# Optimization experiments

Measured on AMD Instinct MI355X. Metric: run time of the kernel, lower is better.

Reference implementation:

```python
import jax, jax.numpy as jnp
import numpy as np

UNITS = 256

def _lstm_step(carry, idx, kernel, rec_kernel, bias, num_chars):
    h, c = carry
    x = jax.nn.one_hot(idx, num_chars, dtype=h.dtype)          # [B, num_chars]
    z = x @ kernel + h @ rec_kernel + bias                      # [B, 4*UNITS]
    i, f, g, o = jnp.split(z, 4, axis=-1)                       # Keras gate order i,f,c,o
    i = jax.nn.sigmoid(i)
    f = jax.nn.sigmoid(f)
    g = jnp.tanh(g)
    o = jax.nn.sigmoid(o)
    c_new = f * c + i * g
    h_new = o * jnp.tanh(c_new)
    return (h_new, c_new), None


def setup_inputs() -> dict:
    key = jax.random.key(0)
    ks = jax.random.split(key, 4)
    num_chars, batch, seq_len = 128, 1024, 512
    x = jax.random.randint(ks[0], (batch, seq_len), 0, num_chars, dtype=jnp.int32)
    kernel = jax.random.normal(ks[1], (num_chars, 4 * UNITS), dtype=jnp.float32) * 0.05
    rec_kernel = jax.random.normal(ks[2], (UNITS, 4 * UNITS), dtype=jnp.float32) * 0.05
    bias = jnp.zeros((4 * UNITS,), dtype=jnp.float32)
    dense_w = jax.random.normal(ks[3], (UNITS, num_chars), dtype=jnp.float32) * 0.05
    dense_b = jnp.zeros((num_chars,), dtype=jnp.float32)
    return {"x": x, "kernel": kernel, "rec_kernel": rec_kernel, "bias": bias,
            "dense_w": dense_w, "dense_b": dense_b}


def reference(x, kernel, rec_kernel, bias, dense_w, dense_b):
    batch = x.shape[0]
    num_chars = kernel.shape[0]
    h0 = jnp.zeros((batch, UNITS), dtype=kernel.dtype)
    c0 = jnp.zeros((batch, UNITS), dtype=kernel.dtype)
    step = lambda carry, idx: _lstm_step(carry, idx, kernel, rec_kernel, bias, num_chars)
    (h, _), _ = jax.lax.scan(step, (h0, c0), x.T)  # scan over time: [S, B]
    logits = h @ dense_w + dense_b                  # [B, num_chars]
    return jax.nn.softmax(logits, axis=-1)
```

## Files before the change

kernel.cpp:

```cpp
#include <hip/hip_runtime.h>
#include <cstdint>

typedef __bf16 bf16x8 __attribute__((ext_vector_type(8)));
typedef float  f32x4  __attribute__((ext_vector_type(4)));

union U4B { uint4 u; bf16x8 b; };
__device__ __forceinline__ bf16x8 as_bf(uint4 u) { U4B x; x.u = u; return x.b; }

__device__ __forceinline__ unsigned short f2b(float x) {
  unsigned int u = __float_as_uint(x);
  unsigned int r = (u + 0x7fffu + ((u >> 16) & 1u)) >> 16;
  return (unsigned short)r;
}
__device__ __forceinline__ float b2f(unsigned int bits_lo16) {
  return __uint_as_float(bits_lo16 << 16);
}

__device__ __forceinline__ float sigm(float x) {
  float e = __builtin_amdgcn_exp2f(x * -1.4426950408889634f);
  return __builtin_amdgcn_rcpf(1.0f + e);
}
__device__ __forceinline__ float tanh_fast(float x) {
  float e = __builtin_amdgcn_exp2f(x * 2.8853900817779268f);
  return 1.0f - 2.0f * __builtin_amdgcn_rcpf(e + 1.0f);
}

__global__ void prep_kernel(const float* __restrict__ rec,
                            const float* __restrict__ kern,
                            const float* __restrict__ bias,
                            const float* __restrict__ dw,
                            unsigned short* __restrict__ recT,
                            unsigned short* __restrict__ kb2,
                            unsigned short* __restrict__ dwT) {
  int id = blockIdx.x * 256 + threadIdx.x;
  if (id < 262144) {
    int colp = id >> 8, k = id & 255;
    int u = colp >> 2, g = colp & 3;
    recT[colp * 256 + k] = f2b(rec[k * 1024 + u + 256 * g]);
  } else if (id < 262144 + 131072) {
    int i = id - 262144;
    int ch = i >> 10, colp = i & 1023;
    int u = colp >> 2, g = colp & 3;
    int oc = u + 256 * g;
    kb2[ch * 1024 + colp] = f2b(kern[ch * 1024 + oc] + bias[oc]);
  } else {
    int i = id - 262144 - 131072;
    int cls = i >> 8, k = i & 255;
    dwT[cls * 256 + k] = f2b(dw[k * 128 + cls]);
  }
}

__global__ __launch_bounds__(512, 2) void lstm_kernel(
    const unsigned short* __restrict__ recT,
    const unsigned short* __restrict__ kb2,
    const unsigned short* __restrict__ dwT,
    const int* __restrict__ x,
    const float* __restrict__ dense_b,
    float* __restrict__ out) {
  __shared__ uint4 A_lds[2][8][512];
  __shared__ unsigned short h_buf[2][16][264];

  const int tid   = threadIdx.x;
  const int lane  = tid & 63;
  const int wid   = tid >> 6;
  const int row16 = lane & 15;
  const int kg    = lane >> 4;
  const int rbase = blockIdx.x << 4;

  const unsigned short* recBase = recT + ((wid * 128 + row16) * 256 + kg * 8);

  uint4 af[4][8];
#pragma unroll
  for (int m = 0; m < 4; ++m)
#pragma unroll
    for (int k = 0; k < 8; ++k) {
      af[m][k] = *(const uint4*)(recBase + m * 4096 + k * 32);
      asm volatile("" : "+v"(af[m][k].x), "+v"(af[m][k].y),
                        "+v"(af[m][k].z), "+v"(af[m][k].w));
    }

#pragma unroll
  for (int s = 0; s < 2; ++s)
#pragma unroll
    for (int k = 0; k < 8; ++k)
      A_lds[s][k][wid * 64 + lane] = *(const uint4*)(recBase + (4 + s) * 4096 + k * 32);

  const unsigned short* sb6 = recBase + 6 * 4096;
  const unsigned short* sb7 = recBase + 7 * 4096;
  uint4 st6[8], st7[8];
#pragma unroll
  for (int k = 0; k < 3; ++k) {
    st6[k] = *(const uint4*)(sb6 + k * 32);
    st7[k] = *(const uint4*)(sb7 + k * 32);
  }

  for (int e = tid; e < 16 * 264; e += 512) (&h_buf[0][0][0])[e] = 0;

  float c_state[8];
#pragma unroll
  for (int m = 0; m < 8; ++m) c_state[m] = 0.0f;

  const int* xrow = x + (rbase + row16) * 512;
  int idx_cur = xrow[0];

  __syncthreads();

  int cur = 0;
  const unsigned aoff_base = (wid * 64 + lane) * 16;

#pragma unroll 1
  for (int t = 0; t < 512; ++t) {
    unsigned z6 = 0, zL = 0;
    asm volatile("" : "+v"(z6), "+v"(zL));
    const unsigned short* sb6v = sb6 + z6;
    const unsigned short* sb7v = sb7 + z6;
    const unsigned aoff = aoff_base + zL;

    int idx_next = xrow[(t + 1 < 512) ? t + 1 : 511];

    const unsigned short* hrow = &h_buf[cur][row16][0];
    const unsigned short* kb = kb2 + (idx_cur * 1024 + wid * 128 + kg * 4);
    uint2 kq[8];

    f32x4 acc[8];
#pragma unroll
    for (int m = 0; m < 8; ++m) acc[m] = f32x4{0.f, 0.f, 0.f, 0.f};

#pragma unroll
    for (int k = 0; k < 8; ++k) {
      uint4 hf = *(const uint4*)(hrow + k * 32 + kg * 8);
      acc[0] = __builtin_amdgcn_mfma_f32_16x16x32_bf16(as_bf(af[0][k]), as_bf(hf), acc[0], 0, 0, 0);
      acc[1] = __builtin_amdgcn_mfma_f32_16x16x32_bf16(as_bf(af[1][k]), as_bf(hf), acc[1], 0, 0, 0);
      acc[2] = __builtin_amdgcn_mfma_f32_16x16x32_bf16(as_bf(af[2][k]), as_bf(hf), acc[2], 0, 0, 0);
      acc[3] = __builtin_amdgcn_mfma_f32_16x16x32_bf16(as_bf(af[3][k]), as_bf(hf), acc[3], 0, 0, 0);
      uint4 a4 = *(const uint4*)((const char*)A_lds + (0 * 8 + k) * 8192 + aoff);
      acc[4] = __builtin_amdgcn_mfma_f32_16x16x32_bf16(as_bf(a4), as_bf(hf), acc[4], 0, 0, 0);
      uint4 a5 = *(const uint4*)((const char*)A_lds + (1 * 8 + k) * 8192 + aoff);
      acc[5] = __builtin_amdgcn_mfma_f32_16x16x32_bf16(as_bf(a5), as_bf(hf), acc[5], 0, 0, 0);
      acc[6] = __builtin_amdgcn_mfma_f32_16x16x32_bf16(as_bf(st6[k]), as_bf(hf), acc[6], 0, 0, 0);
      acc[7] = __builtin_amdgcn_mfma_f32_16x16x32_bf16(as_bf(st7[k]), as_bf(hf), acc[7], 0, 0, 0);
      const int kp = (k + 3) & 7;
      st6[kp] = *(const uint4*)(sb6v + kp * 32);
      st7[kp] = *(const uint4*)(sb7v + kp * 32);
      if (k == 4) {
#pragma unroll
        for (int m = 0; m < 8; ++m) kq[m] = *(const uint2*)(kb + m * 16);
      }
    }

    unsigned short* hn = &h_buf[cur ^ 1][row16][wid * 32 + kg];
#pragma unroll
    for (int m = 0; m < 8; ++m) {
      float zi = acc[m][0] + b2f(kq[m].x & 0xffffu);
      float zf = acc[m][1] + b2f(kq[m].x >> 16);
      float zg = acc[m][2] + b2f(kq[m].y & 0xffffu);
      float zo = acc[m][3] + b2f(kq[m].y >> 16);
      float gi = sigm(zi);
      float gf = sigm(zf);
      float gg = tanh_fast(zg);
      float go = sigm(zo);
      float c  = gf * c_state[m] + gi * gg;
      c_state[m] = c;
      float h  = go * tanh_fast(c);
      hn[m * 4] = f2b(h);
    }
    __syncthreads();
    cur ^= 1;
    idx_cur = idx_next;
  }

  float (*l_lds)[132] = (float (*)[132])A_lds;
  {
    const unsigned short* dwBase = dwT + ((wid * 16 + row16) * 256 + kg * 8);
    uint4 hf[8];
#pragma unroll
    for (int k = 0; k < 8; ++k)
      hf[k] = *(const uint4*)&h_buf[0][row16][k * 32 + kg * 8];
    f32x4 la = {0.f, 0.f, 0.f, 0.f};
#pragma unroll
    for (int k = 0; k < 8; ++k) {
      uint4 afd = *(const uint4*)(dwBase + k * 32);
      la = __builtin_amdgcn_mfma_f32_16x16x32_bf16(as_bf(afd), as_bf(hf[k]), la, 0, 0, 0);
    }
#pragma unroll
    for (int r = 0; r < 4; ++r) {
      int cls = wid * 16 + kg * 4 + r;
      l_lds[row16][cls] = la[r] + dense_b[cls];
    }
  }
  __syncthreads();

  {
    int r = tid >> 5, cg = tid & 31;
    float4 v = *(const float4*)&l_lds[r][cg * 4];
    float mx = fmaxf(fmaxf(v.x, v.y), fmaxf(v.z, v.w));
#pragma unroll
    for (int s = 1; s < 32; s <<= 1) mx = fmaxf(mx, __shfl_xor(mx, s));
    const float L2E = 1.4426950408889634f;
    float e0 = __builtin_amdgcn_exp2f((v.x - mx) * L2E);
    float e1 = __builtin_amdgcn_exp2f((v.y - mx) * L2E);
    float e2 = __builtin_amdgcn_exp2f((v.z - mx) * L2E);
    float e3 = __builtin_amdgcn_exp2f((v.w - mx) * L2E);
    float sm = e0 + e1 + e2 + e3;
#pragma unroll
    for (int s = 1; s < 32; s <<= 1) sm += __shfl_xor(sm, s);
    float inv = __builtin_amdgcn_rcpf(sm);
    float4 o = {e0 * inv, e1 * inv, e2 * inv, e3 * inv};
    *(float4*)&out[(rbase + r) * 128 + cg * 4] = o;
  }
}

extern "C" void kernel_launch(void* const* d_in, const int* in_sizes, int n_in,
                              void* d_out, int out_size, void* d_ws, size_t ws_size,
                              hipStream_t stream) {
  const int*   x      = (const int*)d_in[0];
  const float* kern   = (const float*)d_in[1];
  const float* rec    = (const float*)d_in[2];
  const float* bias   = (const float*)d_in[3];
  const float* dw     = (const float*)d_in[4];
  const float* db     = (const float*)d_in[5];
  float* outp = (float*)d_out;

  unsigned char* ws = (unsigned char*)d_ws;
  unsigned short* recT = (unsigned short*)(ws);
  unsigned short* kb2  = (unsigned short*)(ws + 524288);
  unsigned short* dwT  = (unsigned short*)(ws + 786432);

  prep_kernel<<<1664, 256, 0, stream>>>(rec, kern, bias, dw, recT, kb2, dwT);
  lstm_kernel<<<64, 512, 0, stream>>>(recT, kb2, dwT, x, db, outp);
}
```

Baseline: 2.824 ms.

## Split LSTM step into two half-gate phases overlapping activations with MFMA

Each timestep's gate GEMM is split into two groups of four MFMA accumulators: the first half (register-resident weights) runs, and its gate activations run before the second half (LDS- and streamed weights) is issued, so transcendental work can overlap with matrix work. Input-projection rows for the next timestep are now prefetched a step ahead, and the streamed weight slices are reloaded on a new schedule (upper half at loop top, lower half during the second MFMA phase). Register-resident weights are pinned to AGPRs and the occupancy hint is changed to waves_per_eu(2,2) to relieve VGPR pressure. The result is more live state and a different ordering of global loads that may lengthen the critical dependency chain.

```diff
diff --git a/kernel.cpp b/kernel.cpp
--- a/kernel.cpp
+++ b/kernel.cpp
@@ -50,7 +50,9 @@
   }
 }
 
-__global__ __launch_bounds__(512, 2) void lstm_kernel(
+__global__ __launch_bounds__(512)
+__attribute__((amdgpu_waves_per_eu(2, 2)))
+void lstm_kernel(
     const unsigned short* __restrict__ recT,
     const unsigned short* __restrict__ kb2,
     const unsigned short* __restrict__ dwT,
@@ -75,8 +77,8 @@
 #pragma unroll
     for (int k = 0; k < 8; ++k) {
       af[m][k] = *(const uint4*)(recBase + m * 4096 + k * 32);
-      asm volatile("" : "+v"(af[m][k].x), "+v"(af[m][k].y),
-                        "+v"(af[m][k].z), "+v"(af[m][k].w));
+      asm volatile("" : "+a"(af[m][k].x), "+a"(af[m][k].y),
+                        "+a"(af[m][k].z), "+a"(af[m][k].w));
     }
 
 #pragma unroll
@@ -89,7 +91,7 @@
   const unsigned short* sb7 = recBase + 7 * 4096;
   uint4 st6[8], st7[8];
 #pragma unroll
-  for (int k = 0; k < 3; ++k) {
+  for (int k = 0; k < 4; ++k) {
     st6[k] = *(const uint4*)(sb6 + k * 32);
     st7[k] = *(const uint4*)(sb7 + k * 32);
   }
@@ -102,6 +104,15 @@
 
   const int* xrow = x + (rbase + row16) * 512;
   int idx_cur = xrow[0];
+  const int colb = wid * 128;
+
+  uint2 kq0[4], kq1[4];
+  {
+    const unsigned short* kb = kb2 + (idx_cur * 1024 + colb + kg * 4);
+#pragma unroll
+    for (int m = 0; m < 4; ++m) { kq0[m] = *(const uint2*)(kb + m * 16);
+                                  kq1[m] = *(const uint2*)(kb + (4 + m) * 16); }
+  }
 
   __syncthreads();
 
@@ -116,54 +127,75 @@
     const unsigned short* sb7v = sb7 + z6;
     const unsigned aoff = aoff_base + zL;
 
+#pragma unroll
+    for (int k = 4; k < 8; ++k) {
+      st6[k] = *(const uint4*)(sb6v + k * 32);
+      st7[k] = *(const uint4*)(sb7v + k * 32);
+    }
     int idx_next = xrow[(t + 1 < 512) ? t + 1 : 511];
 
     const unsigned short* hrow = &h_buf[cur][row16][0];
-    const unsigned short* kb = kb2 + (idx_cur * 1024 + wid * 128 + kg * 4);
-    uint2 kq[8];
-
-    f32x4 acc[8];
-#pragma unroll
-    for (int m = 0; m < 8; ++m) acc[m] = f32x4{0.f, 0.f, 0.f, 0.f};
-
+    unsigned short* hn = &h_buf[cur ^ 1][row16][wid * 32 + kg];
+
+    f32x4 a0 = {0,0,0,0}, a1 = {0,0,0,0}, a2 = {0,0,0,0}, a3 = {0,0,0,0};
 #pragma unroll
     for (int k = 0; k < 8; ++k) {
       uint4 hf = *(const uint4*)(hrow + k * 32 + kg * 8);
-      acc[0] = __builtin_amdgcn_mfma_f32_16x16x32_bf16(as_bf(af[0][k]), as_bf(hf), acc[0], 0, 0, 0);
-      acc[1] = __builtin_amdgcn_mfma_f32_16x16x32_bf16(as_bf(af[1][k]), as_bf(hf), acc[1], 0, 0, 0);
-      acc[2] = __builtin_amdgcn_mfma_f32_16x16x32_bf16(as_bf(af[2][k]), as_bf(hf), acc[2], 0, 0, 0);
-      acc[3] = __builtin_amdgcn_mfma_f32_16x16x32_bf16(as_bf(af[3][k]), as_bf(hf), acc[3], 0, 0, 0);
+      a0 = __builtin_amdgcn_mfma_f32_16x16x32_bf16(as_bf(af[0][k]), as_bf(hf), a0, 0, 0, 0);
+      a1 = __builtin_amdgcn_mfma_f32_16x16x32_bf16(as_bf(af[1][k]), as_bf(hf), a1, 0, 0, 0);
+      a2 = __builtin_amdgcn_mfma_f32_16x16x32_bf16(as_bf(af[2][k]), as_bf(hf), a2, 0, 0, 0);
+      a3 = __builtin_amdgcn_mfma_f32_16x16x32_bf16(as_bf(af[3][k]), as_bf(hf), a3, 0, 0, 0);
+    }
+    {
+      f32x4 ag[4] = {a0, a1, a2, a3};
+#pragma unroll
+      for (int m = 0; m < 4; ++m) {
+        float zi = ag[m][0] + b2f(kq0[m].x & 0xffffu);
+        float zf = ag[m][1] + b2f(kq0[m].x >> 16);
+        float zg = ag[m][2] + b2f(kq0[m].y & 0xffffu);
+        float zo = ag[m][3] + b2f(kq0[m].y >> 16);
+        float c  = sigm(zf) * c_state[m] + sigm(zi) * tanh_fast(zg);
+        c_state[m] = c;
+        hn[m * 4] = f2b(sigm(zo) * tanh_fast(c));
+      }
+    }
+
+    const unsigned short* kbn = kb2 + (idx_next * 1024 + colb + kg * 4);
+#pragma unroll
+    for (int m = 0; m < 4; ++m) kq0[m] = *(const uint2*)(kbn + m * 16);
+
+    f32x4 b0 = {0,0,0,0}, b1 = {0,0,0,0}, b2v = {0,0,0,0}, b3 = {0,0,0,0};
+#pragma unroll
+    for (int k = 0; k < 8; ++k) {
+      uint4 hf = *(const uint4*)(hrow + k * 32 + kg * 8);
       uint4 a4 = *(const uint4*)((const char*)A_lds + (0 * 8 + k) * 8192 + aoff);
-      acc[4] = __builtin_amdgcn_mfma_f32_16x16x32_bf16(as_bf(a4), as_bf(hf), acc[4], 0, 0, 0);
       uint4 a5 = *(const uint4*)((const char*)A_lds + (1 * 8 + k) * 8192 + aoff);
-      acc[5] = __builtin_amdgcn_mfma_f32_16x16x32_bf16(as_bf(a5), as_bf(hf), acc[5], 0, 0, 0);
-      acc[6] = __builtin_amdgcn_mfma_f32_16x16x32_bf16(as_bf(st6[k]), as_bf(hf), acc[6], 0, 0, 0);
-      acc[7] = __builtin_amdgcn_mfma_f32_16x16x32_bf16(as_bf(st7[k]), as_bf(hf), acc[7], 0, 0, 0);
-      const int kp = (k + 3) & 7;
-      st6[kp] = *(const uint4*)(sb6v + kp * 32);
-      st7[kp] = *(const uint4*)(sb7v + kp * 32);
-      if (k == 4) {
-#pragma unroll
-        for (int m = 0; m < 8; ++m) kq[m] = *(const uint2*)(kb + m * 16);
+      b0 = __builtin_amdgcn_mfma_f32_16x16x32_bf16(as_bf(a4), as_bf(hf), b0, 0, 0, 0);
+      b1 = __builtin_amdgcn_mfma_f32_16x16x32_bf16(as_bf(a5), as_bf(hf), b1, 0, 0, 0);
+      b2v = __builtin_amdgcn_mfma_f32_16x16x32_bf16(as_bf(st6[k]), as_bf(hf), b2v, 0, 0, 0);
+      b3 = __builtin_amdgcn_mfma_f32_16x16x32_bf16(as_bf(st7[k]), as_bf(hf), b3, 0, 0, 0);
+      if (k < 4) {
+        st6[k] = *(const uint4*)(sb6v + k * 32);
+        st7[k] = *(const uint4*)(sb7v + k * 32);
       }
     }
-
-    unsigned short* hn = &h_buf[cur ^ 1][row16][wid * 32 + kg];
-#pragma unroll
-    for (int m = 0; m < 8; ++m) {
-      float zi = acc[m][0] + b2f(kq[m].x & 0xffffu);
-      float zf = acc[m][1] + b2f(kq[m].x >> 16);
-      float zg = acc[m][2] + b2f(kq[m].y & 0xffffu);
-      float zo = acc[m][3] + b2f(kq[m].y >> 16);
-      float gi = sigm(zi);
-      float gf = sigm(zf);
-      float gg = tanh_fast(zg);
-      float go = sigm(zo);
-      float c  = gf * c_state[m] + gi * gg;
-      c_state[m] = c;
-      float h  = go * tanh_fast(c);
-      hn[m * 4] = f2b(h);
-    }
+    {
+      f32x4 bg[4] = {b0, b1, b2v, b3};
+#pragma unroll
+      for (int m = 0; m < 4; ++m) {
+        float zi = bg[m][0] + b2f(kq1[m].x & 0xffffu);
+        float zf = bg[m][1] + b2f(kq1[m].x >> 16);
+        float zg = bg[m][2] + b2f(kq1[m].y & 0xffffu);
+        float zo = bg[m][3] + b2f(kq1[m].y >> 16);
+        float c  = sigm(zf) * c_state[4 + m] + sigm(zi) * tanh_fast(zg);
+        c_state[4 + m] = c;
+        hn[(4 + m) * 4] = f2b(sigm(zo) * tanh_fast(c));
+      }
+    }
+
+#pragma unroll
+    for (int m = 0; m < 4; ++m) kq1[m] = *(const uint2*)(kbn + (4 + m) * 16);
+
     __syncthreads();
     cur ^= 1;
     idx_cur = idx_next;
@@ -172,15 +204,12 @@
   float (*l_lds)[132] = (float (*)[132])A_lds;
   {
     const unsigned short* dwBase = dwT + ((wid * 16 + row16) * 256 + kg * 8);
-    uint4 hf[8];
-#pragma unroll
-    for (int k = 0; k < 8; ++k)
-      hf[k] = *(const uint4*)&h_buf[0][row16][k * 32 + kg * 8];
     f32x4 la = {0.f, 0.f, 0.f, 0.f};
 #pragma unroll
     for (int k = 0; k < 8; ++k) {
+      uint4 hf  = *(const uint4*)&h_buf[0][row16][k * 32 + kg * 8];
       uint4 afd = *(const uint4*)(dwBase + k * 32);
-      la = __builtin_amdgcn_mfma_f32_16x16x32_bf16(as_bf(afd), as_bf(hf[k]), la, 0, 0, 0);
+      la = __builtin_amdgcn_mfma_f32_16x16x32_bf16(as_bf(afd), as_bf(hf), la, 0, 0, 0);
     }
 #pragma unroll
     for (int r = 0; r < 4; ++r) {
@@ -195,7 +224,7 @@
     float4 v = *(const float4*)&l_lds[r][cg * 4];
     float mx = fmaxf(fmaxf(v.x, v.y), fmaxf(v.z, v.w));
 #pragma unroll
-    for (int s = 1; s < 32; s <<= 1) mx = fmaxf(mx, __shfl_xor(mx, s));
+    for (int sh = 1; sh < 32; sh <<= 1) mx = fmaxf(mx, __shfl_xor(mx, sh));
     const float L2E = 1.4426950408889634f;
     float e0 = __builtin_amdgcn_exp2f((v.x - mx) * L2E);
     float e1 = __builtin_amdgcn_exp2f((v.y - mx) * L2E);
@@ -203,7 +232,7 @@
     float e3 = __builtin_amdgcn_exp2f((v.w - mx) * L2E);
     float sm = e0 + e1 + e2 + e3;
 #pragma unroll
-    for (int s = 1; s < 32; s <<= 1) sm += __shfl_xor(sm, s);
+    for (int sh = 1; sh < 32; sh <<= 1) sm += __shfl_xor(sm, sh);
     float inv = __builtin_amdgcn_rcpf(sm);
     float4 o = {e0 * inv, e1 * inv, e2 * inv, e3 * inv};
     *(float4*)&out[(rbase + r) * 128 + cg * 4] = o;
```

Result: no change. 2.784 ms (-1.4%).
